# Optimization experiments

Measured on AMD Instinct MI355X. Metric: run time of the kernel, lower is better.

## Reference

```python
import math
import jax, jax.numpy as jnp
import numpy as np

HEAD_SIZE = 64
DEPTH = 0

def lambda_init_fn(depth):
    depth = depth + 1
    return 0.8 - 0.6 * math.exp(-0.3 * depth)

def setup_inputs() -> dict:
    key = jax.random.key(0)
    ks = jax.random.split(key, 9)
    B, T, C = 4, 4096, 1024
    H2 = 2 * HEAD_SIZE  # 128
    return {
        "x":  jax.random.normal(ks[0], (B, T, C), dtype=jnp.float32),
        "Wq": jax.random.normal(ks[1], (C, H2), dtype=jnp.float32) * (C ** -0.5),
        "Wk": jax.random.normal(ks[2], (C, H2), dtype=jnp.float32) * (C ** -0.5),
        "Wv": jax.random.normal(ks[3], (C, H2), dtype=jnp.float32) * (C ** -0.5),
        "lambda_q1": jax.random.normal(ks[4], (HEAD_SIZE,), dtype=jnp.float32) * 0.1,
        "lambda_q2": jax.random.normal(ks[5], (HEAD_SIZE,), dtype=jnp.float32) * 0.1,
        "lambda_k1": jax.random.normal(ks[6], (HEAD_SIZE,), dtype=jnp.float32) * 0.1,
        "lambda_k2": jax.random.normal(ks[7], (HEAD_SIZE,), dtype=jnp.float32) * 0.1,
    }

def reference(x, Wq, Wk, Wv, lambda_q1, lambda_q2, lambda_k1, lambda_k2):
    B, T, C = x.shape
    q = x @ Wq  # (B,T,2*hs)
    k = x @ Wk
    v = x @ Wv  # (B,T,2*hs)
    q1, q2 = jnp.split(q, 2, axis=-1)
    k1, k2 = jnp.split(k, 2, axis=-1)
    scale = 1.0 / math.sqrt(HEAD_SIZE)
    w1 = jnp.einsum('btd,bsd->bts', q1, k1) * scale  # (B,T,T)
    w2 = jnp.einsum('btd,bsd->bts', q2, k2) * scale
    causal = jnp.tril(jnp.ones((T, T), dtype=bool))
    neg_inf = jnp.float32(-jnp.inf)
    w1 = jnp.where(causal, w1, neg_inf)
    w2 = jnp.where(causal, w2, neg_inf)
    lam1 = jnp.exp(jnp.sum(lambda_q1 * lambda_k1))
    lam2 = jnp.exp(jnp.sum(lambda_q2 * lambda_k2))
    lam = lam1 - lam2 + lambda_init_fn(DEPTH)
    weights = jax.nn.softmax(w1, axis=-1) - lam * jax.nn.softmax(w2, axis=-1)
    out = jnp.einsum('bts,bsd->btd', weights, v)  # (B,T,2*hs)
    return out
```

## Files before the change

kernel.cpp:

```cpp
#include <hip/hip_runtime.h>
#include <hip/hip_bf16.h>

typedef __bf16 bf16x8 __attribute__((ext_vector_type(8)));
typedef float f32x4 __attribute__((ext_vector_type(4)));

#define LOG2E 1.4426950408889634f
#define LAMBDA_INIT 0.3555090675909693f
#define CEXP 0.18033688011112042f
#define MOFF 11.541560327111708f

#define K_OFF   ((size_t)16384 * 128)
#define VT_OFF  ((size_t)2 * 16384 * 128)
#define PART_OFF_BYTES ((size_t)12582912)
#define REC_FLOATS 4160

__device__ __forceinline__ unsigned short f2bf(float f) {
    __hip_bfloat16 h = __float2bfloat16(f);
    unsigned short u;
    __builtin_memcpy(&u, &h, 2);
    return u;
}
__device__ __forceinline__ float bf2f(unsigned short u) {
    unsigned int x = ((unsigned int)u) << 16;
    float f;
    __builtin_memcpy(&f, &x, 4);
    return f;
}
__device__ __forceinline__ unsigned int cvt_pk_bf16(float a, float b) {
    unsigned int r;
    asm volatile("v_cvt_pk_bf16_f32 %0, %1, %2" : "=v"(r) : "v"(a), "v"(b));
    return r;
}

__global__ __launch_bounds__(256) void prep_wt(
    const float* __restrict__ Wq, const float* __restrict__ Wk,
    const float* __restrict__ Wv, unsigned short* __restrict__ WT) {
    const int kt = blockIdx.x, nt = blockIdx.y, mat = blockIdx.z;
    const float* W = (mat == 0) ? Wq : (mat == 1) ? Wk : Wv;
    unsigned short* O = WT + (size_t)mat * 128 * 1024;
    __shared__ float tb[64][65];
    const int r = threadIdx.x >> 2, c4 = (threadIdx.x & 3) * 16;
    for (int j = 0; j < 4; ++j) {
        float4 v = *(const float4*)&W[(size_t)(kt * 64 + r) * 128 + nt * 64 + c4 + j * 4];
        tb[r][c4 + j * 4 + 0] = v.x;
        tb[r][c4 + j * 4 + 1] = v.y;
        tb[r][c4 + j * 4 + 2] = v.z;
        tb[r][c4 + j * 4 + 3] = v.w;
    }
    __syncthreads();
    unsigned short tmp[16];
    for (int j = 0; j < 16; ++j) tmp[j] = f2bf(tb[c4 + j][r]);
    *(uint4*)&O[(size_t)(nt * 64 + r) * 1024 + kt * 64 + c4] = *(uint4*)&tmp[0];
    *(uint4*)&O[(size_t)(nt * 64 + r) * 1024 + kt * 64 + c4 + 8] = *(uint4*)&tmp[8];
}

__global__ __launch_bounds__(256) void qkv_gemm(
    const float* __restrict__ x, const unsigned short* __restrict__ WT,
    unsigned short* __restrict__ qkv) {
    const int tid = threadIdx.x;
    const int l = tid & 63, wid = tid >> 6;
    const int g = l >> 4, i16 = l & 15;
    const int row0 = blockIdx.x * 128;
    const int mat = blockIdx.y;
    const unsigned short* Wt = WT + (size_t)mat * 128 * 1024;

    __shared__ unsigned short smem[2][128][72];
    auto xs = smem[0];
    auto wt = smem[1];

    f32x4 acc[2][8];
    const f32x4 z4 = {0.f, 0.f, 0.f, 0.f};
    for (int a = 0; a < 2; ++a)
        for (int b = 0; b < 8; ++b) acc[a][b] = z4;

    for (int k0 = 0; k0 < 1024; k0 += 64) {
        __syncthreads();
        {
            const int c = (tid & 15) * 4;
            const int rbase = tid >> 4;
            #pragma unroll
            for (int it = 0; it < 8; ++it) {
                int r = rbase + it * 16;
                const float4 v = *(const float4*)&x[(size_t)(row0 + r) * 1024 + k0 + c];
                ushort4 pk = make_ushort4(f2bf(v.x), f2bf(v.y), f2bf(v.z), f2bf(v.w));
                *(ushort4*)&xs[r][c] = pk;
            }
        }
        {
            #pragma unroll
            for (int it = 0; it < 4; ++it) {
                int lin = it * 256 + tid;
                int n = lin >> 3, k8 = (lin & 7) * 8;
                *(uint4*)&wt[n][k8] = *(const uint4*)&Wt[(size_t)n * 1024 + k0 + k8];
            }
        }
        __syncthreads();

        bf16x8 af[2][2];
        for (int rb = 0; rb < 2; ++rb)
            for (int c = 0; c < 2; ++c)
                af[rb][c] = *(const bf16x8*)&xs[wid * 32 + rb * 16 + i16][c * 32 + 8 * g];
        for (int nb = 0; nb < 8; ++nb) {
            bf16x8 b0 = *(const bf16x8*)&wt[nb * 16 + i16][8 * g];
            bf16x8 b1 = *(const bf16x8*)&wt[nb * 16 + i16][32 + 8 * g];
            for (int rb = 0; rb < 2; ++rb) {
                acc[rb][nb] = __builtin_amdgcn_mfma_f32_16x16x32_bf16(af[rb][0], b0, acc[rb][nb], 0, 0, 0);
                acc[rb][nb] = __builtin_amdgcn_mfma_f32_16x16x32_bf16(af[rb][1], b1, acc[rb][nb], 0, 0, 0);
            }
        }
    }

    __syncthreads();
    unsigned short(*ts)[136] = (unsigned short(*)[136]) & smem[0][0][0];
    for (int rb = 0; rb < 2; ++rb)
        for (int nb = 0; nb < 8; ++nb)
            for (int r = 0; r < 4; ++r)
                ts[wid * 32 + rb * 16 + g * 4 + r][nb * 16 + i16] = f2bf(acc[rb][nb][r]);
    __syncthreads();

    const int bq = row0 >> 12;
    const int s0b = (row0 & 4095) >> 6;
    if (mat == 0) {
        unsigned short* outp = qkv + (size_t)row0 * 128;
        #pragma unroll
        for (int it = 0; it < 8; ++it) {
            int tr = it * 16 + (tid >> 4), dv0 = (tid & 15) * 8;
            *(uint4*)&outp[tr * 128 + dv0] = *(const uint4*)&ts[tr][dv0];
        }
    } else if (mat == 1) {
        unsigned short* kimg = qkv + K_OFF;
        #pragma unroll
        for (int it = 0; it < 8; ++it) {
            int lin = it * 256 + tid;
            int tile = lin >> 10;
            int branch_ = (lin >> 9) & 1;
            int region = (lin >> 6) & 7;
            int slot = lin & 63;
            int row = tile * 64 + (region >> 1) * 16 + (slot & 15);
            int d = branch_ * 64 + (region & 1) * 32 + (slot >> 4) * 8;
            uint4 vv = *(const uint4*)&ts[row][d];
            size_t off = ((size_t)((bq * 64 + s0b + tile) * 2 + branch_) * 4096) + (region * 64 + slot) * 8;
            *(uint4*)&kimg[off] = vv;
        }
    } else {
        unsigned short* vimg = qkv + VT_OFF;
        #pragma unroll
        for (int it = 0; it < 8; ++it) {
            int lin = it * 256 + tid;
            int tile = lin >> 10;
            int rem = lin & 1023;
            int region = rem >> 6;
            int slot = rem & 63;
            int dv = (region >> 1) * 16 + (slot & 15);
            int kv0 = (region & 1) * 32 + (slot >> 4) * 8;
            unsigned short tmp[8];
            #pragma unroll
            for (int e = 0; e < 8; ++e) tmp[e] = ts[tile * 64 + kv0 + e][dv];
            size_t off = ((size_t)(bq * 64 + s0b + tile) * 8192) + (region * 64 + slot) * 8;
            *(uint4*)&vimg[off] = *(uint4*)tmp;
        }
    }
}

__global__ __launch_bounds__(256, 3) void diff_attn_pair(
    const unsigned short* __restrict__ q, const unsigned short* __restrict__ kimg,
    const unsigned short* __restrict__ vimg,
    float* __restrict__ part, int ncs) {
    const int bx = blockIdx.x, b = blockIdx.y;
    const int c = blockIdx.z >> 1, branch = blockIdx.z & 1;
    const int bxe = (c & 1) ? (31 - bx) : bx;
    const int t_o = 63 - 2 * bxe, t_e = t_o - 1;
    const int n = t_o + 1;
    const int s_lo = (c * n) >> ncs, smax = ((c + 1) * n) >> ncs;

    if (s_lo >= smax) return;

    const int tid = threadIdx.x;
    const int l = tid & 63, w = tid >> 6;
    const int gq = l >> 4, i16 = l & 15;
    const float NEGINF = -__builtin_inff();

    __shared__ unsigned short ksf[4096];
    __shared__ unsigned short psf[8192];

    float* recA = part + ((((size_t)(b * 64 + t_e) << ncs) + c) * 2 + branch) * REC_FLOATS;
    float* recB = part + ((((size_t)(b * 64 + t_o) << ncs) + c) * 2 + branch) * REC_FLOATS;
    const bool emptyA = (s_lo > t_e);

    const size_t bbase = (size_t)b * 4096;
    const unsigned short* kimg_b = kimg + (size_t)b * 524288;
    const unsigned short* vimg_b = vimg + (size_t)b * 524288;
    const int tid8 = tid * 8;
    const int l8 = l * 8;
    const f32x4 z4 = {0.f, 0.f, 0.f, 0.f};

    bf16x8 qfA[2], qfB[2];
    #pragma unroll
    for (int cc = 0; cc < 2; ++cc) {
        qfA[cc] = *(const bf16x8*)&q[(bbase + t_e * 64 + w * 16 + i16) * 128 + branch * 64 + cc * 32 + 8 * gq];
        qfB[cc] = *(const bf16x8*)&q[(bbase + t_o * 64 + w * 16 + i16) * 128 + branch * 64 + cc * 32 + 8 * gq];
    }

    float lsumA = 0.f, lsumB = 0.f;
    f32x4 acc[2][4][2];
    for (int qs = 0; qs < 2; ++qs)
        for (int qg = 0; qg < 4; ++qg)
            for (int j = 0; j < 2; ++j) acc[qs][qg][j] = z4;

    int pdst[4];
    #pragma unroll
    for (int cb = 0; cb < 4; ++cb)
        pdst[cb] = ((w * 2 + (cb >> 1)) * 64 + ((cb & 1) * 2 + (gq >> 1)) * 16 + i16) * 8 + (gq & 1) * 4;

    uint4 kr0, kr1;
    bf16x8 vb00, vb01, vb10, vb11;

#define K_ISSUE(s_) do {                                                            \
        const unsigned short* kp = &kimg_b[((size_t)(s_) * 2 + branch) * 4096];     \
        kr0 = *(const uint4*)&kp[tid8];                                             \
        kr1 = *(const uint4*)&kp[tid8 + 2048];                                      \
    } while (0)
#define V_ISSUE(s_) do {                                                            \
        const unsigned short* vp = &vimg_b[(size_t)(s_) * 8192 + w * 2048];         \
        vb00 = *(const bf16x8*)&vp[l8];                                             \
        vb01 = *(const bf16x8*)&vp[512 + l8];                                       \
        vb10 = *(const bf16x8*)&vp[1024 + l8];                                      \
        vb11 = *(const bf16x8*)&vp[1536 + l8];                                      \
    } while (0)

    K_ISSUE(s_lo);
    V_ISSUE(s_lo);
    #pragma unroll 1
    for (int s = s_lo; s < smax; ++s) {
        __syncthreads();
        *(uint4*)&ksf[tid8] = kr0;
        *(uint4*)&ksf[tid8 + 2048] = kr1;
        if (s + 1 < smax) K_ISSUE(s + 1);
        __syncthreads();
        const bool aAct = (s != t_o);

        if (aAct) {
            f32x4 sc[4];
            for (int cb = 0; cb < 4; ++cb) sc[cb] = z4;
            __builtin_amdgcn_s_setprio(1);
            #pragma unroll
            for (int cb = 0; cb < 4; ++cb)
                for (int cc = 0; cc < 2; ++cc) {
                    bf16x8 kf = *(const bf16x8*)&ksf[((cb * 2 + cc) * 64 + l) * 8];
                    sc[cb] = __builtin_amdgcn_mfma_f32_16x16x32_bf16(kf, qfA[cc], sc[cb], 0, 0, 0);
                }
            __builtin_amdgcn_s_setprio(0);
            if (s == t_e) {
                int ql = w * 16 + i16;
                for (int cb = 0; cb < 4; ++cb)
                    for (int r = 0; r < 4; ++r)
                        if (cb * 16 + gq * 4 + r > ql) sc[cb][r] = NEGINF;
            }
            #pragma unroll
            for (int cb = 0; cb < 4; ++cb) {
                float p0 = exp2f(fmaf(sc[cb][0], CEXP, -MOFF));
                float p1 = exp2f(fmaf(sc[cb][1], CEXP, -MOFF));
                float p2 = exp2f(fmaf(sc[cb][2], CEXP, -MOFF));
                float p3 = exp2f(fmaf(sc[cb][3], CEXP, -MOFF));
                lsumA += (p0 + p1) + (p2 + p3);
                uint2 pw;
                pw.x = cvt_pk_bf16(p0, p1);
                pw.y = cvt_pk_bf16(p2, p3);
                *(uint2*)&psf[pdst[cb]] = pw;
            }
        }
        {
            f32x4 sc[4];
            for (int cb = 0; cb < 4; ++cb) sc[cb] = z4;
            __builtin_amdgcn_s_setprio(1);
            #pragma unroll
            for (int cb = 0; cb < 4; ++cb)
                for (int cc = 0; cc < 2; ++cc) {
                    bf16x8 kf = *(const bf16x8*)&ksf[((cb * 2 + cc) * 64 + l) * 8];
                    sc[cb] = __builtin_amdgcn_mfma_f32_16x16x32_bf16(kf, qfB[cc], sc[cb], 0, 0, 0);
                }
            __builtin_amdgcn_s_setprio(0);
            if (s == t_o) {
                int ql = w * 16 + i16;
                for (int cb = 0; cb < 4; ++cb)
                    for (int r = 0; r < 4; ++r)
                        if (cb * 16 + gq * 4 + r > ql) sc[cb][r] = NEGINF;
            }
            #pragma unroll
            for (int cb = 0; cb < 4; ++cb) {
                float p0 = exp2f(fmaf(sc[cb][0], CEXP, -MOFF));
                float p1 = exp2f(fmaf(sc[cb][1], CEXP, -MOFF));
                float p2 = exp2f(fmaf(sc[cb][2], CEXP, -MOFF));
                float p3 = exp2f(fmaf(sc[cb][3], CEXP, -MOFF));
                lsumB += (p0 + p1) + (p2 + p3);
                uint2 pw;
                pw.x = cvt_pk_bf16(p0, p1);
                pw.y = cvt_pk_bf16(p2, p3);
                *(uint2*)&psf[4096 + pdst[cb]] = pw;
            }
        }
        __syncthreads();

        __builtin_amdgcn_s_setprio(1);
        if (aAct) {
            #pragma unroll
            for (int qg = 0; qg < 4; ++qg) {
                bf16x8 pa0 = *(const bf16x8*)&psf[(qg * 2 + 0) * 512 + l8];
                bf16x8 pa1 = *(const bf16x8*)&psf[(qg * 2 + 1) * 512 + l8];
                acc[0][qg][0] = __builtin_amdgcn_mfma_f32_16x16x32_bf16(pa0, vb00, acc[0][qg][0], 0, 0, 0);
                acc[0][qg][0] = __builtin_amdgcn_mfma_f32_16x16x32_bf16(pa1, vb01, acc[0][qg][0], 0, 0, 0);
                acc[0][qg][1] = __builtin_amdgcn_mfma_f32_16x16x32_bf16(pa0, vb10, acc[0][qg][1], 0, 0, 0);
                acc[0][qg][1] = __builtin_amdgcn_mfma_f32_16x16x32_bf16(pa1, vb11, acc[0][qg][1], 0, 0, 0);
            }
        }
        #pragma unroll
        for (int qg = 0; qg < 4; ++qg) {
            bf16x8 pa0 = *(const bf16x8*)&psf[4096 + (qg * 2 + 0) * 512 + l8];
            bf16x8 pa1 = *(const bf16x8*)&psf[4096 + (qg * 2 + 1) * 512 + l8];
            acc[1][qg][0] = __builtin_amdgcn_mfma_f32_16x16x32_bf16(pa0, vb00, acc[1][qg][0], 0, 0, 0);
            acc[1][qg][0] = __builtin_amdgcn_mfma_f32_16x16x32_bf16(pa1, vb01, acc[1][qg][0], 0, 0, 0);
            acc[1][qg][1] = __builtin_amdgcn_mfma_f32_16x16x32_bf16(pa0, vb10, acc[1][qg][1], 0, 0, 0);
            acc[1][qg][1] = __builtin_amdgcn_mfma_f32_16x16x32_bf16(pa1, vb11, acc[1][qg][1], 0, 0, 0);
        }
        __builtin_amdgcn_s_setprio(0);
        if (s + 1 < smax) V_ISSUE(s + 1);
    }
#undef K_ISSUE
#undef V_ISSUE

    lsumA += __shfl_xor(lsumA, 16);
    lsumA += __shfl_xor(lsumA, 32);
    lsumB += __shfl_xor(lsumB, 16);
    lsumB += __shfl_xor(lsumB, 32);
    if (!emptyA) {
        if (gq == 0) recA[w * 16 + i16] = lsumA;
        unsigned short* OA = (unsigned short*)(recA + 64);
        for (int qg = 0; qg < 4; ++qg)
            for (int j = 0; j < 2; ++j)
                for (int r = 0; r < 4; ++r)
                    OA[(qg * 16 + gq * 4 + r) * 128 + (w * 2 + j) * 16 + i16] = f2bf(acc[0][qg][j][r]);
    }
    {
        if (gq == 0) recB[w * 16 + i16] = lsumB;
        unsigned short* OB = (unsigned short*)(recB + 64);
        for (int qg = 0; qg < 4; ++qg)
            for (int j = 0; j < 2; ++j)
                for (int r = 0; r < 4; ++r)
                    OB[(qg * 16 + gq * 4 + r) * 128 + (w * 2 + j) * 16 + i16] = f2bf(acc[1][qg][j][r]);
    }
}

__global__ __launch_bounds__(256) void diff_combine(
    const float* __restrict__ part,
    const float* __restrict__ lq1, const float* __restrict__ lq2,
    const float* __restrict__ lk1, const float* __restrict__ lk2,
    float* __restrict__ out, int ncs) {
    const int t = blockIdx.x, b = blockIdx.y;
    const int tid = threadIdx.x;
    const int nc = 1 << ncs;
    const int n = (t | 1) + 1;
    __shared__ float sl[2][64];
    __shared__ float s_lam;

    const float* recbase = part + (((size_t)(b * 64 + t) << ncs)) * 2 * REC_FLOATS;

    if (tid < 64) {
        float s1 = lq1[tid] * lk1[tid];
        float s2 = lq2[tid] * lk2[tid];
        for (int off = 32; off > 0; off >>= 1) {
            s1 += __shfl_xor(s1, off);
            s2 += __shfl_xor(s2, off);
        }
        if (tid == 0) s_lam = expf(s1) - expf(s2) + LAMBDA_INIT;
    }
    if (tid < 128) {
        int r = tid & 63, br = tid >> 6;
        float acc = 0.f;
        for (int c = 0; c < nc; ++c) {
            int lo = (c * n) >> ncs, hi = ((c + 1) * n) >> ncs;
            if (lo >= hi || lo > t) continue;
            acc += recbase[(c * 2 + br) * REC_FLOATS + r];
        }
        sl[br][r] = acc;
    }
    __syncthreads();
    const float lam = s_lam;

    float* op = out + ((size_t)b * 4096 + (size_t)t * 64) * 128;
    for (int grp = 0; grp < 4; ++grp) {
        int gid = grp * 256 + tid;
        int e = gid * 8;
        int row = e >> 7;
        float o1[8] = {0, 0, 0, 0, 0, 0, 0, 0}, o2[8] = {0, 0, 0, 0, 0, 0, 0, 0};
        for (int c = 0; c < nc; ++c) {
            int lo = (c * n) >> ncs, hi = ((c + 1) * n) >> ncs;
            if (lo >= hi || lo > t) continue;
            const unsigned short* O0 = (const unsigned short*)(recbase + (c * 2 + 0) * REC_FLOATS + 64);
            const unsigned short* O1 = (const unsigned short*)(recbase + (c * 2 + 1) * REC_FLOATS + 64);
            uint4 u0 = *(const uint4*)&O0[e];
            uint4 u1 = *(const uint4*)&O1[e];
            const unsigned short* e0 = (const unsigned short*)&u0;
            const unsigned short* e1 = (const unsigned short*)&u1;
            #pragma unroll
            for (int j = 0; j < 8; ++j) {
                o1[j] += bf2f(e0[j]);
                o2[j] += bf2f(e1[j]);
            }
        }
        float l1inv = 1.0f / sl[0][row], l2inv = 1.0f / sl[1][row];
        float res[8];
        #pragma unroll
        for (int j = 0; j < 8; ++j) res[j] = o1[j] * l1inv - lam * o2[j] * l2inv;
        *(float4*)&op[e] = *(float4*)&res[0];
        *(float4*)&op[e + 4] = *(float4*)&res[4];
    }
}

extern "C" void kernel_launch(void* const* d_in, const int* in_sizes, int n_in,
                              void* d_out, int out_size, void* d_ws, size_t ws_size,
                              hipStream_t stream) {
    const float* x   = (const float*)d_in[0];
    const float* Wq  = (const float*)d_in[1];
    const float* Wk  = (const float*)d_in[2];
    const float* Wv  = (const float*)d_in[3];
    const float* lq1 = (const float*)d_in[4];
    const float* lq2 = (const float*)d_in[5];
    const float* lk1 = (const float*)d_in[6];
    const float* lk2 = (const float*)d_in[7];
    float* out = (float*)d_out;
    unsigned short* qkv = (unsigned short*)d_ws;

    const size_t WT_BYTES = (size_t)3 * 128 * 1024 * 2;
    int ncs = 2;
    {
        size_t part8 = (size_t)256 * 8 * 2 * REC_FLOATS * 4;
        if (ws_size >= PART_OFF_BYTES + part8 + WT_BYTES) ncs = 3;
    }
    const size_t part_bytes = (size_t)256 * (1 << ncs) * 2 * REC_FLOATS * 4;
    float* part = (float*)((char*)d_ws + PART_OFF_BYTES);
    unsigned short* WT = (unsigned short*)((char*)d_ws + PART_OFF_BYTES + part_bytes);

    prep_wt<<<dim3(16, 2, 3), 256, 0, stream>>>(Wq, Wk, Wv, WT);
    qkv_gemm<<<dim3(128, 3), 256, 0, stream>>>(x, WT, qkv);

    const unsigned short* qb = qkv;
    const unsigned short* kb = qkv + K_OFF;
    const unsigned short* vtb = qkv + VT_OFF;
    diff_attn_pair<<<dim3(32, 4, 2 << ncs), 256, 0, stream>>>(qb, kb, vtb, part, ncs);
    diff_combine<<<dim3(64, 4), 256, 0, stream>>>(part, lq1, lq2, lk1, lk2, out, ncs);
}
```

Measured before the change: 102.2 us.

## Shrink QKV GEMM tiles, fold softmax scale into Q, fix split count

The QKV projection GEMM now uses 64-row tiles with one 16-row slab per wave, doubling the grid to 768 blocks so more CUs are busy. The softmax exponent scale CEXP is multiplied into Q before it is stored as bf16, so the attention inner loop calls exp2f on raw scores without an fma or the fixed max offset. The key-split count is pinned at 4 instead of choosing 8 when the workspace is large enough. Costs: each block reloads the full W tile for half as many rows, rounding Q after scaling changes numerics slightly, dropping the offset raises overflow risk on large scores, and a smaller split count may leave the attention kernel with less parallelism.

```diff
diff --git a/kernel.cpp b/kernel.cpp
--- a/kernel.cpp
+++ b/kernel.cpp
@@ -4,10 +4,8 @@
 typedef __bf16 bf16x8 __attribute__((ext_vector_type(8)));
 typedef float f32x4 __attribute__((ext_vector_type(4)));
 
-#define LOG2E 1.4426950408889634f
 #define LAMBDA_INIT 0.3555090675909693f
 #define CEXP 0.18033688011112042f
-#define MOFF 11.541560327111708f
 
 #define K_OFF   ((size_t)16384 * 128)
 #define VT_OFF  ((size_t)2 * 16384 * 128)
@@ -58,29 +56,27 @@
     const float* __restrict__ x, const unsigned short* __restrict__ WT,
     unsigned short* __restrict__ qkv) {
     const int tid = threadIdx.x;
-    const int l = tid & 63, wid = tid >> 6;
+    const int l = tid & 63, w = tid >> 6;
     const int g = l >> 4, i16 = l & 15;
-    const int row0 = blockIdx.x * 128;
+    const int row0 = blockIdx.x * 64;
     const int mat = blockIdx.y;
     const unsigned short* Wt = WT + (size_t)mat * 128 * 1024;
 
-    __shared__ unsigned short smem[2][128][72];
-    auto xs = smem[0];
-    auto wt = smem[1];
-
-    f32x4 acc[2][8];
+    __shared__ unsigned short xs[64][72];
+    __shared__ unsigned short wt[128][72];
+
+    f32x4 acc[8];
     const f32x4 z4 = {0.f, 0.f, 0.f, 0.f};
-    for (int a = 0; a < 2; ++a)
-        for (int b = 0; b < 8; ++b) acc[a][b] = z4;
+    for (int nb = 0; nb < 8; ++nb) acc[nb] = z4;
 
     for (int k0 = 0; k0 < 1024; k0 += 64) {
         __syncthreads();
         {
             const int c = (tid & 15) * 4;
-            const int rbase = tid >> 4;
-            #pragma unroll
-            for (int it = 0; it < 8; ++it) {
-                int r = rbase + it * 16;
+            const int rb = tid >> 4;
+            #pragma unroll
+            for (int it = 0; it < 4; ++it) {
+                int r = (rb + it * 16) & 63;
                 const float4 v = *(const float4*)&x[(size_t)(row0 + r) * 1024 + k0 + c];
                 ushort4 pk = make_ushort4(f2bf(v.x), f2bf(v.y), f2bf(v.z), f2bf(v.w));
                 *(ushort4*)&xs[r][c] = pk;
@@ -96,68 +92,60 @@
         }
         __syncthreads();
 
-        bf16x8 af[2][2];
-        for (int rb = 0; rb < 2; ++rb)
-            for (int c = 0; c < 2; ++c)
-                af[rb][c] = *(const bf16x8*)&xs[wid * 32 + rb * 16 + i16][c * 32 + 8 * g];
+        bf16x8 af0 = *(const bf16x8*)&xs[w * 16 + i16][8 * g];
+        bf16x8 af1 = *(const bf16x8*)&xs[w * 16 + i16][32 + 8 * g];
+        #pragma unroll
         for (int nb = 0; nb < 8; ++nb) {
             bf16x8 b0 = *(const bf16x8*)&wt[nb * 16 + i16][8 * g];
             bf16x8 b1 = *(const bf16x8*)&wt[nb * 16 + i16][32 + 8 * g];
-            for (int rb = 0; rb < 2; ++rb) {
-                acc[rb][nb] = __builtin_amdgcn_mfma_f32_16x16x32_bf16(af[rb][0], b0, acc[rb][nb], 0, 0, 0);
-                acc[rb][nb] = __builtin_amdgcn_mfma_f32_16x16x32_bf16(af[rb][1], b1, acc[rb][nb], 0, 0, 0);
-            }
+            acc[nb] = __builtin_amdgcn_mfma_f32_16x16x32_bf16(af0, b0, acc[nb], 0, 0, 0);
+            acc[nb] = __builtin_amdgcn_mfma_f32_16x16x32_bf16(af1, b1, acc[nb], 0, 0, 0);
         }
     }
 
     __syncthreads();
-    unsigned short(*ts)[136] = (unsigned short(*)[136]) & smem[0][0][0];
-    for (int rb = 0; rb < 2; ++rb)
-        for (int nb = 0; nb < 8; ++nb)
-            for (int r = 0; r < 4; ++r)
-                ts[wid * 32 + rb * 16 + g * 4 + r][nb * 16 + i16] = f2bf(acc[rb][nb][r]);
+    unsigned short(*ts)[136] = (unsigned short(*)[136]) & wt[0][0];
+    const float qscale = (mat == 0) ? CEXP : 1.0f;
+    for (int nb = 0; nb < 8; ++nb)
+        for (int r = 0; r < 4; ++r)
+            ts[w * 16 + g * 4 + r][nb * 16 + i16] = f2bf(acc[nb][r] * qscale);
     __syncthreads();
 
     const int bq = row0 >> 12;
-    const int s0b = (row0 & 4095) >> 6;
+    const int s = (row0 >> 6) & 63;
     if (mat == 0) {
         unsigned short* outp = qkv + (size_t)row0 * 128;
         #pragma unroll
-        for (int it = 0; it < 8; ++it) {
+        for (int it = 0; it < 4; ++it) {
             int tr = it * 16 + (tid >> 4), dv0 = (tid & 15) * 8;
             *(uint4*)&outp[tr * 128 + dv0] = *(const uint4*)&ts[tr][dv0];
         }
     } else if (mat == 1) {
-        unsigned short* kimg = qkv + K_OFF;
-        #pragma unroll
-        for (int it = 0; it < 8; ++it) {
+        unsigned short* kimg = qkv + K_OFF + ((size_t)(bq * 64 + s) * 2) * 4096;
+        #pragma unroll
+        for (int it = 0; it < 4; ++it) {
             int lin = it * 256 + tid;
-            int tile = lin >> 10;
             int branch_ = (lin >> 9) & 1;
             int region = (lin >> 6) & 7;
             int slot = lin & 63;
-            int row = tile * 64 + (region >> 1) * 16 + (slot & 15);
+            int row = (region >> 1) * 16 + (slot & 15);
             int d = branch_ * 64 + (region & 1) * 32 + (slot >> 4) * 8;
             uint4 vv = *(const uint4*)&ts[row][d];
-            size_t off = ((size_t)((bq * 64 + s0b + tile) * 2 + branch_) * 4096) + (region * 64 + slot) * 8;
-            *(uint4*)&kimg[off] = vv;
+            *(uint4*)&kimg[(size_t)branch_ * 4096 + (region * 64 + slot) * 8] = vv;
         }
     } else {
-        unsigned short* vimg = qkv + VT_OFF;
-        #pragma unroll
-        for (int it = 0; it < 8; ++it) {
+        unsigned short* vimg = qkv + VT_OFF + (size_t)(bq * 64 + s) * 8192;
+        #pragma unroll
+        for (int it = 0; it < 4; ++it) {
             int lin = it * 256 + tid;
-            int tile = lin >> 10;
-            int rem = lin & 1023;
-            int region = rem >> 6;
-            int slot = rem & 63;
+            int region = lin >> 6;
+            int slot = lin & 63;
             int dv = (region >> 1) * 16 + (slot & 15);
             int kv0 = (region & 1) * 32 + (slot >> 4) * 8;
             unsigned short tmp[8];
             #pragma unroll
-            for (int e = 0; e < 8; ++e) tmp[e] = ts[tile * 64 + kv0 + e][dv];
-            size_t off = ((size_t)(bq * 64 + s0b + tile) * 8192) + (region * 64 + slot) * 8;
-            *(uint4*)&vimg[off] = *(uint4*)tmp;
+            for (int e = 0; e < 8; ++e) tmp[e] = ts[kv0 + e][dv];
+            *(uint4*)&vimg[(region * 64 + slot) * 8] = *(uint4*)tmp;
         }
     }
 }
@@ -258,10 +246,10 @@
             }
             #pragma unroll
             for (int cb = 0; cb < 4; ++cb) {
-                float p0 = exp2f(fmaf(sc[cb][0], CEXP, -MOFF));
-                float p1 = exp2f(fmaf(sc[cb][1], CEXP, -MOFF));
-                float p2 = exp2f(fmaf(sc[cb][2], CEXP, -MOFF));
-                float p3 = exp2f(fmaf(sc[cb][3], CEXP, -MOFF));
+                float p0 = exp2f(sc[cb][0]);
+                float p1 = exp2f(sc[cb][1]);
+                float p2 = exp2f(sc[cb][2]);
+                float p3 = exp2f(sc[cb][3]);
                 lsumA += (p0 + p1) + (p2 + p3);
                 uint2 pw;
                 pw.x = cvt_pk_bf16(p0, p1);
@@ -288,10 +276,10 @@
             }
             #pragma unroll
             for (int cb = 0; cb < 4; ++cb) {
-                float p0 = exp2f(fmaf(sc[cb][0], CEXP, -MOFF));
-                float p1 = exp2f(fmaf(sc[cb][1], CEXP, -MOFF));
-                float p2 = exp2f(fmaf(sc[cb][2], CEXP, -MOFF));
-                float p3 = exp2f(fmaf(sc[cb][3], CEXP, -MOFF));
+                float p0 = exp2f(sc[cb][0]);
+                float p1 = exp2f(sc[cb][1]);
+                float p2 = exp2f(sc[cb][2]);
+                float p3 = exp2f(sc[cb][3]);
                 lsumB += (p0 + p1) + (p2 + p3);
                 uint2 pw;
                 pw.x = cvt_pk_bf16(p0, p1);
@@ -430,18 +418,13 @@
     float* out = (float*)d_out;
     unsigned short* qkv = (unsigned short*)d_ws;
 
-    const size_t WT_BYTES = (size_t)3 * 128 * 1024 * 2;
-    int ncs = 2;
-    {
-        size_t part8 = (size_t)256 * 8 * 2 * REC_FLOATS * 4;
-        if (ws_size >= PART_OFF_BYTES + part8 + WT_BYTES) ncs = 3;
-    }
+    const int ncs = 2;
     const size_t part_bytes = (size_t)256 * (1 << ncs) * 2 * REC_FLOATS * 4;
     float* part = (float*)((char*)d_ws + PART_OFF_BYTES);
     unsigned short* WT = (unsigned short*)((char*)d_ws + PART_OFF_BYTES + part_bytes);
 
     prep_wt<<<dim3(16, 2, 3), 256, 0, stream>>>(Wq, Wk, Wv, WT);
-    qkv_gemm<<<dim3(128, 3), 256, 0, stream>>>(x, WT, qkv);
+    qkv_gemm<<<dim3(256, 3), 256, 0, stream>>>(x, WT, qkv);
 
     const unsigned short* qb = qkv;
     const unsigned short* kb = qkv + K_OFF;
```

New measurement: 119.4 us. +16.9%, slower.
